# Kernel tuning notes

Hardware: AMD Instinct MI355X
Metric: run time of the kernel (lower is better)

## Reference

```python
import jax, jax.numpy as jnp
import numpy as np

B = 4096
IN_FEATS = 1024
OUT_FEATS = 1024
NUM_HEADS = 16
NUM_MEMS = 4096
HEAD_DIM = OUT_FEATS // NUM_HEADS
TEMPERATURE = 1.0
EPS = 0.0  # original code uses plain jnp.linalg.norm (no eps)


def setup_inputs() -> dict:
    key = jax.random.key(0)
    k1, k2, k3 = jax.random.split(key, 3)
    x = jax.random.normal(k1, (B, IN_FEATS), dtype=jnp.float32)
    # eqx.nn.Linear stores weight as [out, in]; uniform-like init replaced with normal scaled
    W_q = jax.random.normal(k2, (OUT_FEATS, IN_FEATS), dtype=jnp.float32) * (1.0 / np.sqrt(IN_FEATS))
    memories = jax.random.normal(k3, (NUM_HEADS, NUM_MEMS, HEAD_DIM), dtype=jnp.float32) * 0.02
    return {"x": x, "W_q": W_q, "memories": memories}


def reference(x, W_q, memories):
    # q = query_proj(x): [B, out_feats] -> [B, H, d]
    q = (x @ W_q.T).reshape(B, NUM_HEADS, HEAD_DIM)
    # L2-normalize queries and memories along feature dim
    q_norm = q / jnp.linalg.norm(q, axis=-1, keepdims=True)
    mem_norm = memories / jnp.linalg.norm(memories, axis=-1, keepdims=True)
    # cosine-similarity scores: [B, H, M]
    attn_scores = jnp.einsum('bhd,hmd->bhm', q_norm, mem_norm)
    # soft readout (hard=False branch)
    mem_probs = jax.nn.softmax(attn_scores / TEMPERATURE, axis=-1)
    # weighted combine of normalized memories, scaled by sqrt(head_dim)
    out = jnp.einsum('bhm,hmd->bhd', mem_probs, mem_norm) * jnp.sqrt(HEAD_DIM).astype(x.dtype)
    return out.reshape(B, OUT_FEATS)
```

## Files before the change

### kernel.cpp

```cpp
#include <hip/hip_runtime.h>
#include <stdint.h>

#define B_SZ  4096
#define HEADS 16
#define HD    64
#define M_SZ  4096
#define K_IN  1024
#define SW    72
#define LOG2E 1.44269504088896f

typedef _Float16 f16;
typedef f16  f16x2 __attribute__((ext_vector_type(2)));
typedef f16  f16x4 __attribute__((ext_vector_type(4)));
typedef f16  f16x8 __attribute__((ext_vector_type(8)));
typedef float f32x4 __attribute__((ext_vector_type(4)));

union U8 { uint4 u4; f16x8 h8; unsigned int ui[4]; unsigned short us[8]; };

__device__ __forceinline__ unsigned short f2h(float f) {
    _Float16 h = (_Float16)f;
    return __builtin_bit_cast(unsigned short, h);
}
__device__ __forceinline__ f16x8 ldsv8(const unsigned short* p) {
    U8 u; u.u4 = *reinterpret_cast<const uint4*>(p); return u.h8;
}

#if __has_builtin(__builtin_amdgcn_exp2f)
#define EXP2F(x) __builtin_amdgcn_exp2f(x)
#else
#define EXP2F(x) __expf((x) * 0.6931471805599453f)
#endif

__device__ __forceinline__ void gload_lds16(const void* g, void* l) {
    __builtin_amdgcn_global_load_lds(
        (const __attribute__((address_space(1))) void*)g,
        (__attribute__((address_space(3))) void*)l, 16, 0, 0);
}

__global__ __launch_bounds__(256) void k_conv(const float* __restrict__ x,
                                              const float* __restrict__ Wq,
                                              unsigned short* __restrict__ xh,
                                              unsigned short* __restrict__ Wh) {
    const int b = blockIdx.x;
    const float* src;
    unsigned short* dst;
    size_t base;
    if (b < 2048) { src = x;  dst = xh; base = (size_t)b * 2048; }
    else          { src = Wq; dst = Wh; base = (size_t)(b - 2048) * 2048; }
    const size_t i = base + (size_t)threadIdx.x * 8;
    float4 f0 = reinterpret_cast<const float4*>(src + i)[0];
    float4 f1 = reinterpret_cast<const float4*>(src + i)[1];
    U8 u;
    u.us[0] = f2h(f0.x); u.us[1] = f2h(f0.y); u.us[2] = f2h(f0.z); u.us[3] = f2h(f0.w);
    u.us[4] = f2h(f1.x); u.us[5] = f2h(f1.y); u.us[6] = f2h(f1.z); u.us[7] = f2h(f1.w);
    *reinterpret_cast<uint4*>(dst + i) = u.u4;
}

__global__ __launch_bounds__(256) void k_prep_mem(const float* __restrict__ mem,
                                                  unsigned short* __restrict__ F) {
    __shared__ float part[64][4];
    __shared__ float scale[64];
    __shared__ unsigned short Tn[64 * SW];

    const int h  = blockIdx.y;
    const int tl = blockIdx.x;
    const int m0 = tl * 64;
    const int tid = threadIdx.x;
    const int r = tid >> 2;
    const int c = tid & 3;

    const float* src = mem + ((size_t)(h * M_SZ + m0 + r)) * HD + c * 16;
    float v[16];
    float ss = 0.f;
#pragma unroll
    for (int i = 0; i < 4; i++) {
        float4 f = reinterpret_cast<const float4*>(src)[i];
        v[4*i+0] = f.x; v[4*i+1] = f.y; v[4*i+2] = f.z; v[4*i+3] = f.w;
        ss += f.x*f.x + f.y*f.y + f.z*f.z + f.w*f.w;
    }
    part[r][c] = ss;
    __syncthreads();
    if (tid < 64) {
        float s = part[tid][0] + part[tid][1] + part[tid][2] + part[tid][3];
        scale[tid] = rsqrtf(s);
    }
    __syncthreads();
    const float sc = scale[r];

    U8 a, b;
#pragma unroll
    for (int i = 0; i < 8; i++) { a.us[i] = f2h(v[i] * sc); b.us[i] = f2h(v[8 + i] * sc); }
    *reinterpret_cast<uint4*>(&Tn[r * SW + c * 16])     = a.u4;
    *reinterpret_cast<uint4*>(&Tn[r * SW + c * 16 + 8]) = b.u4;
    __syncthreads();

    const int w = tid >> 6, lane = tid & 63;
    const int l15 = lane & 15, quad = lane >> 4;
    unsigned short* Fd = F + ((size_t)(h * 64 + tl) * 16) * 512;

#pragma unroll
    for (int i = 0; i < 2; i++) {
        const int ch = w * 2 + i, g = ch >> 1, s = ch & 1;
        const int mp = 32 * (g >> 1) + ((l15 >> 2) * 8) + 4 * (g & 1) + (l15 & 3);
        uint4 vv = *reinterpret_cast<const uint4*>(&Tn[mp * SW + s * 32 + quad * 8]);
        *reinterpret_cast<uint4*>(Fd + ch * 512 + lane * 8) = vv;
    }
#pragma unroll
    for (int i = 0; i < 2; i++) {
        const int c2 = w * 2 + i, p = c2 >> 2, n = c2 & 3;
        U8 u;
#pragma unroll
        for (int j = 0; j < 8; j++)
            u.us[j] = Tn[(32 * p + quad * 8 + j) * SW + n * 16 + l15];
        *reinterpret_cast<uint4*>(Fd + (8 + c2) * 512 + lane * 8) = u.u4;
    }
}

__global__ __launch_bounds__(256, 2) void k_qproj(const unsigned short* __restrict__ xh,
                                                  const unsigned short* __restrict__ Wh,
                                                  unsigned short* __restrict__ qn) {
    __shared__ unsigned short As[128 * SW];
    __shared__ unsigned short Bs[64 * SW];

    const int b0 = blockIdx.x * 128;
    const int n0 = blockIdx.y * 64;
    const int t = threadIdx.x;
    const int w = t >> 6, lane = t & 63;
    const int l15 = lane & 15, quad = lane >> 4;

    f32x4 acc[2][4] = {};

    for (int kb = 0; kb < K_IN; kb += 64) {
        __syncthreads();
        {
            const unsigned short* px = xh + (size_t)(b0 + (t >> 1)) * K_IN + kb + (t & 1) * 32;
            const unsigned short* pw = Wh + (size_t)(n0 + (t >> 2)) * K_IN + kb + (t & 3) * 16;
            uint4 av[4];
#pragma unroll
            for (int i = 0; i < 4; i++) av[i] = reinterpret_cast<const uint4*>(px)[i];
            uint4 bv[2];
#pragma unroll
            for (int i = 0; i < 2; i++) bv[i] = reinterpret_cast<const uint4*>(pw)[i];
#pragma unroll
            for (int i = 0; i < 4; i++)
                *reinterpret_cast<uint4*>(&As[(t >> 1) * SW + (t & 1) * 32 + i * 8]) = av[i];
#pragma unroll
            for (int i = 0; i < 2; i++)
                *reinterpret_cast<uint4*>(&Bs[(t >> 2) * SW + (t & 3) * 16 + i * 8]) = bv[i];
        }
        __syncthreads();

#pragma unroll
        for (int s = 0; s < 2; s++) {
            f16x8 af[2];
#pragma unroll
            for (int qg = 0; qg < 2; qg++)
                af[qg] = ldsv8(&As[(w * 32 + qg * 16 + l15) * SW + s * 32 + quad * 8]);
#pragma unroll
            for (int g = 0; g < 4; g++) {
                f16x8 bf_ = ldsv8(&Bs[(g * 16 + l15) * SW + s * 32 + quad * 8]);
#pragma unroll
                for (int qg = 0; qg < 2; qg++)
                    acc[qg][g] = __builtin_amdgcn_mfma_f32_16x16x32_f16(af[qg], bf_, acc[qg][g], 0, 0, 0);
            }
        }
    }

    __syncthreads();
    unsigned short* Ct = As;
#pragma unroll
    for (int qg = 0; qg < 2; qg++) {
        float ssq[4];
#pragma unroll
        for (int r = 0; r < 4; r++) {
            float s = 0.f;
#pragma unroll
            for (int g = 0; g < 4; g++) s += acc[qg][g][r] * acc[qg][g][r];
            ssq[r] = s;
        }
#pragma unroll
        for (int mask = 1; mask <= 8; mask <<= 1)
#pragma unroll
            for (int r = 0; r < 4; r++) ssq[r] += __shfl_xor(ssq[r], mask, 64);
#pragma unroll
        for (int r = 0; r < 4; r++) {
            float inv = rsqrtf(ssq[r]) * LOG2E;
#pragma unroll
            for (int g = 0; g < 4; g++)
                Ct[(w * 32 + qg * 16 + quad * 4 + r) * SW + g * 16 + l15] = f2h(acc[qg][g][r] * inv);
        }
    }
    __syncthreads();

    const int row = t >> 1, half = (t & 1) * 32;
    unsigned short* dq = qn + (size_t)(b0 + row) * 1024 + n0 + half;
#pragma unroll
    for (int i = 0; i < 4; i++)
        reinterpret_cast<uint4*>(dq)[i] = *reinterpret_cast<const uint4*>(&Ct[row * SW + half + i * 8]);
}

__global__ __launch_bounds__(256, 2) void k_attn(const unsigned short* __restrict__ qn,
                                                 const unsigned short* __restrict__ F,
                                                 float* __restrict__ out) {
    __shared__ unsigned short buf[4][8192];

    const int b = blockIdx.x;
    const int h  = 2 * (b & 7) + (b >> 8);
    const int b0 = ((b >> 3) & 31) * 128;
    const int t = threadIdx.x;
    const int w = t >> 6, lane = t & 63;
    const int l15 = lane & 15, quad = lane >> 4;

    const f32x4 Z = {0.f, 0.f, 0.f, 0.f};

    f16x8 qf[2][2];
#pragma unroll
    for (int qg = 0; qg < 2; qg++)
#pragma unroll
        for (int s = 0; s < 2; s++) {
            U8 u;
            u.u4 = *reinterpret_cast<const uint4*>(
                qn + (size_t)(b0 + w * 32 + qg * 16 + l15) * 1024 + h * 64 + s * 32 + quad * 8);
            qf[qg][s] = u.h8;
        }

    const unsigned short* Fh = F + (size_t)h * 64 * 8192;

    f32x4 accO[2][4] = {};
    float lsum[2] = {0.f, 0.f};

    f16x8 puA[2][2], puB[2][2];
    f16x8 bwA[8],   bwB[8];

#if __has_builtin(__builtin_amdgcn_fdot2)
    const f16x2 one2 = {(_Float16)1.f, (_Float16)1.f};
#define LSUM4(qgi, puv)                                                          \
    {                                                                            \
        float s_ = lsum[qgi];                                                    \
        s_ = __builtin_amdgcn_fdot2(__builtin_bit_cast(f16x2, (puv).ui[0]), one2, s_, false); \
        s_ = __builtin_amdgcn_fdot2(__builtin_bit_cast(f16x2, (puv).ui[1]), one2, s_, false); \
        s_ = __builtin_amdgcn_fdot2(__builtin_bit_cast(f16x2, (puv).ui[2]), one2, s_, false); \
        s_ = __builtin_amdgcn_fdot2(__builtin_bit_cast(f16x2, (puv).ui[3]), one2, s_, false); \
        lsum[qgi] = s_;                                                          \
    }
#else
#define LSUM4(qgi, puv)                                                          \
    {                                                                            \
        float a0 = (float)(puv).h8[0] + (float)(puv).h8[1];                      \
        float a1 = (float)(puv).h8[2] + (float)(puv).h8[3];                      \
        float a2 = (float)(puv).h8[4] + (float)(puv).h8[5];                      \
        float a3 = (float)(puv).h8[6] + (float)(puv).h8[7];                      \
        lsum[qgi] += (a0 + a1) + (a2 + a3);                                      \
    }
#endif

#pragma unroll
    for (int tp = 0; tp < 3; tp++)
#pragma unroll
        for (int i = 0; i < 4; i++) {
            const int ch = w * 4 + i;
            gload_lds16(Fh + (size_t)tp * 8192 + ch * 512 + lane * 8, &buf[tp][ch * 512]);
        }
    __syncthreads();
    {
        f16x8 am[8];
#pragma unroll
        for (int ch = 0; ch < 8; ch++) am[ch] = ldsv8(&buf[0][ch * 512 + lane * 8]);
#pragma unroll
        for (int ch = 0; ch < 8; ch++) bwA[ch] = ldsv8(&buf[0][(8 + ch) * 512 + lane * 8]);
#pragma unroll
        for (int g = 0; g < 4; g++) {
            const int qg = g >> 1, p = g & 1;
            f32x4 t0 = __builtin_amdgcn_mfma_f32_16x16x32_f16(am[4*p+0], qf[qg][0], Z, 0, 0, 0);
            t0 = __builtin_amdgcn_mfma_f32_16x16x32_f16(am[4*p+1], qf[qg][1], t0, 0, 0, 0);
            f32x4 t1 = __builtin_amdgcn_mfma_f32_16x16x32_f16(am[4*p+2], qf[qg][0], Z, 0, 0, 0);
            t1 = __builtin_amdgcn_mfma_f32_16x16x32_f16(am[4*p+3], qf[qg][1], t1, 0, 0, 0);
            float p0 = EXP2F(t0[0]), p1 = EXP2F(t0[1]), p2 = EXP2F(t0[2]), p3 = EXP2F(t0[3]);
            float p4 = EXP2F(t1[0]), p5 = EXP2F(t1[1]), p6 = EXP2F(t1[2]), p7 = EXP2F(t1[3]);
            U8 pu;
#if __has_builtin(__builtin_amdgcn_cvt_pkrtz)
            pu.ui[0] = __builtin_bit_cast(unsigned int, __builtin_amdgcn_cvt_pkrtz(p0, p1));
            pu.ui[1] = __builtin_bit_cast(unsigned int, __builtin_amdgcn_cvt_pkrtz(p2, p3));
            pu.ui[2] = __builtin_bit_cast(unsigned int, __builtin_amdgcn_cvt_pkrtz(p4, p5));
            pu.ui[3] = __builtin_bit_cast(unsigned int, __builtin_amdgcn_cvt_pkrtz(p6, p7));
#else
            pu.us[0]=f2h(p0); pu.us[1]=f2h(p1); pu.us[2]=f2h(p2); pu.us[3]=f2h(p3);
            pu.us[4]=f2h(p4); pu.us[5]=f2h(p5); pu.us[6]=f2h(p6); pu.us[7]=f2h(p7);
#endif
            LSUM4(qg, pu);
            puA[qg][p] = pu.h8;
        }
    }

    auto body = [&](int tl, f16x8 (&puC)[2][2], f16x8 (&bwC)[8],
                            f16x8 (&puN)[2][2], f16x8 (&bwN)[8]) {
        const unsigned short* lb = buf[(tl + 1) & 3];
        f16x8 amn[8];
#pragma unroll
        for (int ch = 0; ch < 8; ch++) amn[ch] = ldsv8(&lb[ch * 512 + lane * 8]);
#pragma unroll
        for (int ch = 0; ch < 8; ch++) bwN[ch] = ldsv8(&lb[(8 + ch) * 512 + lane * 8]);
        if (tl + 3 < 64) {
            const unsigned short* gsrc = Fh + (size_t)(tl + 3) * 8192;
#pragma unroll
            for (int i = 0; i < 4; i++) {
                const int ch = w * 4 + i;
                gload_lds16(gsrc + ch * 512 + lane * 8, &buf[(tl + 3) & 3][ch * 512]);
            }
        }

        f32x4 sa[4], sb[4];
        auto expPack = [&](int g) {
            const int qg = g >> 1, p = g & 1;
            float p0 = EXP2F(sa[g][0]), p1 = EXP2F(sa[g][1]), p2 = EXP2F(sa[g][2]), p3 = EXP2F(sa[g][3]);
            float p4 = EXP2F(sb[g][0]), p5 = EXP2F(sb[g][1]), p6 = EXP2F(sb[g][2]), p7 = EXP2F(sb[g][3]);
            U8 pu;
#if __has_builtin(__builtin_amdgcn_cvt_pkrtz)
            pu.ui[0] = __builtin_bit_cast(unsigned int, __builtin_amdgcn_cvt_pkrtz(p0, p1));
            pu.ui[1] = __builtin_bit_cast(unsigned int, __builtin_amdgcn_cvt_pkrtz(p2, p3));
            pu.ui[2] = __builtin_bit_cast(unsigned int, __builtin_amdgcn_cvt_pkrtz(p4, p5));
            pu.ui[3] = __builtin_bit_cast(unsigned int, __builtin_amdgcn_cvt_pkrtz(p6, p7));
#else
            pu.us[0]=f2h(p0); pu.us[1]=f2h(p1); pu.us[2]=f2h(p2); pu.us[3]=f2h(p3);
            pu.us[4]=f2h(p4); pu.us[5]=f2h(p5); pu.us[6]=f2h(p6); pu.us[7]=f2h(p7);
#endif
            LSUM4(qg, pu);
            puN[qg][p] = pu.h8;
        };

#pragma unroll
        for (int g = 0; g < 4; g++) {
            const int qg = g >> 1, p = g & 1;
            __builtin_amdgcn_s_setprio(1);
            f32x4 t0 = __builtin_amdgcn_mfma_f32_16x16x32_f16(amn[4*p+0], qf[qg][0], Z, 0, 0, 0);
            t0 = __builtin_amdgcn_mfma_f32_16x16x32_f16(amn[4*p+1], qf[qg][1], t0, 0, 0, 0);
            f32x4 t1 = __builtin_amdgcn_mfma_f32_16x16x32_f16(amn[4*p+2], qf[qg][0], Z, 0, 0, 0);
            t1 = __builtin_amdgcn_mfma_f32_16x16x32_f16(amn[4*p+3], qf[qg][1], t1, 0, 0, 0);
            sa[g] = t0; sb[g] = t1;
#pragma unroll
            for (int n = 0; n < 4; n++)
                accO[qg][n] = __builtin_amdgcn_mfma_f32_16x16x32_f16(puC[qg][p], bwC[p * 4 + n], accO[qg][n], 0, 0, 0);
            __builtin_amdgcn_s_setprio(0);
            if (g >= 1) expPack(g - 1);
        }
        expPack(3);
    };

    for (int tt = 0; tt < 31; ++tt) {
        __syncthreads();
        body(2 * tt,     puA, bwA, puB, bwB);
        body(2 * tt + 1, puB, bwB, puA, bwA);
    }
    __syncthreads();
    body(62, puA, bwA, puB, bwB);

#pragma unroll
    for (int g = 0; g < 4; g++) {
        const int qg = g >> 1, p = g & 1;
#pragma unroll
        for (int n = 0; n < 4; n++)
            accO[qg][n] = __builtin_amdgcn_mfma_f32_16x16x32_f16(puB[qg][p], bwB[p * 4 + n], accO[qg][n], 0, 0, 0);
    }

#pragma unroll
    for (int qg = 0; qg < 2; qg++) {
        float s = lsum[qg];
        s += __shfl_xor(s, 16, 64);
        s += __shfl_xor(s, 32, 64);
        float inv = 8.0f / s;
#pragma unroll
        for (int r = 0; r < 4; r++) {
            float iv = __shfl(inv, quad * 4 + r, 64);
            float* po = out + (size_t)(b0 + w * 32 + qg * 16 + quad * 4 + r) * 1024 + h * 64;
#pragma unroll
            for (int n = 0; n < 4; n++)
                po[n * 16 + l15] = accO[qg][n][r] * iv;
        }
    }
}

extern "C" void kernel_launch(void* const* d_in, const int* in_sizes, int n_in,
                              void* d_out, int out_size, void* d_ws, size_t ws_size,
                              hipStream_t stream) {
    (void)in_sizes; (void)n_in; (void)out_size; (void)ws_size;
    const float* x   = (const float*)d_in[0];
    const float* Wq  = (const float*)d_in[1];
    const float* mem = (const float*)d_in[2];
    float* out = (float*)d_out;

    unsigned short* qn = (unsigned short*)d_ws;
    unsigned short* F  = qn + (size_t)B_SZ * 1024;
    unsigned short* xh = F  + (size_t)HEADS * 64 * 16 * 512;
    unsigned short* Wh = xh + (size_t)B_SZ * K_IN;

    k_conv    <<<2560, 256, 0, stream>>>(x, Wq, xh, Wh);
    k_prep_mem<<<dim3(64, 16), 256, 0, stream>>>(mem, F);
    k_qproj   <<<dim3(32, 16), 256, 0, stream>>>(xh, Wh, qn);
    k_attn    <<<512, 256, 0, stream>>>(qn, F, out);
}
```

Before: 175.3 us.

## Fuse fp16 conversion into qproj and merge memory prep into one launch

Removes the separate fp32-to-fp16 conversion kernel by having the query-projection GEMM load fp32 x and W_q directly and pack to fp16 while staging into LDS. Memory normalization blocks and qproj blocks are merged into a single launch using block-index ranges, cutting two launches and the intermediate xh/Wh round trip through global memory. The GEMM now reads twice the bytes per tile from global memory (fp32) and does conversion per tile, and W_q is re-converted by every row block.

```diff
diff --git a/kernel.cpp b/kernel.cpp
--- a/kernel.cpp
+++ b/kernel.cpp
@@ -31,100 +31,94 @@
 #define EXP2F(x) __expf((x) * 0.6931471805599453f)
 #endif
 
+#if __has_builtin(__builtin_amdgcn_cvt_pkrtz)
+#define PK2(a, b) __builtin_bit_cast(unsigned int, __builtin_amdgcn_cvt_pkrtz((a), (b)))
+#else
+__device__ __forceinline__ unsigned int PK2(float a, float b) {
+    return (unsigned int)f2h(a) | ((unsigned int)f2h(b) << 16);
+}
+#endif
+
 __device__ __forceinline__ void gload_lds16(const void* g, void* l) {
     __builtin_amdgcn_global_load_lds(
         (const __attribute__((address_space(1))) void*)g,
         (__attribute__((address_space(3))) void*)l, 16, 0, 0);
 }
 
-__global__ __launch_bounds__(256) void k_conv(const float* __restrict__ x,
-                                              const float* __restrict__ Wq,
-                                              unsigned short* __restrict__ xh,
-                                              unsigned short* __restrict__ Wh) {
+__global__ __launch_bounds__(256, 2) void k_fused(const float* __restrict__ x,
+                                                  const float* __restrict__ Wq,
+                                                  const float* __restrict__ mem,
+                                                  unsigned short* __restrict__ F,
+                                                  unsigned short* __restrict__ qn) {
+    __shared__ __align__(16) unsigned char smem[27648];
     const int b = blockIdx.x;
-    const float* src;
-    unsigned short* dst;
-    size_t base;
-    if (b < 2048) { src = x;  dst = xh; base = (size_t)b * 2048; }
-    else          { src = Wq; dst = Wh; base = (size_t)(b - 2048) * 2048; }
-    const size_t i = base + (size_t)threadIdx.x * 8;
-    float4 f0 = reinterpret_cast<const float4*>(src + i)[0];
-    float4 f1 = reinterpret_cast<const float4*>(src + i)[1];
-    U8 u;
-    u.us[0] = f2h(f0.x); u.us[1] = f2h(f0.y); u.us[2] = f2h(f0.z); u.us[3] = f2h(f0.w);
-    u.us[4] = f2h(f1.x); u.us[5] = f2h(f1.y); u.us[6] = f2h(f1.z); u.us[7] = f2h(f1.w);
-    *reinterpret_cast<uint4*>(dst + i) = u.u4;
-}
-
-__global__ __launch_bounds__(256) void k_prep_mem(const float* __restrict__ mem,
-                                                  unsigned short* __restrict__ F) {
-    __shared__ float part[64][4];
-    __shared__ float scale[64];
-    __shared__ unsigned short Tn[64 * SW];
-
-    const int h  = blockIdx.y;
-    const int tl = blockIdx.x;
-    const int m0 = tl * 64;
-    const int tid = threadIdx.x;
-    const int r = tid >> 2;
-    const int c = tid & 3;
-
-    const float* src = mem + ((size_t)(h * M_SZ + m0 + r)) * HD + c * 16;
-    float v[16];
-    float ss = 0.f;
-#pragma unroll
-    for (int i = 0; i < 4; i++) {
-        float4 f = reinterpret_cast<const float4*>(src)[i];
-        v[4*i+0] = f.x; v[4*i+1] = f.y; v[4*i+2] = f.z; v[4*i+3] = f.w;
-        ss += f.x*f.x + f.y*f.y + f.z*f.z + f.w*f.w;
-    }
-    part[r][c] = ss;
-    __syncthreads();
-    if (tid < 64) {
-        float s = part[tid][0] + part[tid][1] + part[tid][2] + part[tid][3];
-        scale[tid] = rsqrtf(s);
-    }
-    __syncthreads();
-    const float sc = scale[r];
-
-    U8 a, b;
-#pragma unroll
-    for (int i = 0; i < 8; i++) { a.us[i] = f2h(v[i] * sc); b.us[i] = f2h(v[8 + i] * sc); }
-    *reinterpret_cast<uint4*>(&Tn[r * SW + c * 16])     = a.u4;
-    *reinterpret_cast<uint4*>(&Tn[r * SW + c * 16 + 8]) = b.u4;
-    __syncthreads();
-
-    const int w = tid >> 6, lane = tid & 63;
-    const int l15 = lane & 15, quad = lane >> 4;
-    unsigned short* Fd = F + ((size_t)(h * 64 + tl) * 16) * 512;
-
-#pragma unroll
-    for (int i = 0; i < 2; i++) {
-        const int ch = w * 2 + i, g = ch >> 1, s = ch & 1;
-        const int mp = 32 * (g >> 1) + ((l15 >> 2) * 8) + 4 * (g & 1) + (l15 & 3);
-        uint4 vv = *reinterpret_cast<const uint4*>(&Tn[mp * SW + s * 32 + quad * 8]);
-        *reinterpret_cast<uint4*>(Fd + ch * 512 + lane * 8) = vv;
-    }
-#pragma unroll
-    for (int i = 0; i < 2; i++) {
-        const int c2 = w * 2 + i, p = c2 >> 2, n = c2 & 3;
-        U8 u;
-#pragma unroll
-        for (int j = 0; j < 8; j++)
-            u.us[j] = Tn[(32 * p + quad * 8 + j) * SW + n * 16 + l15];
-        *reinterpret_cast<uint4*>(Fd + (8 + c2) * 512 + lane * 8) = u.u4;
-    }
-}
-
-__global__ __launch_bounds__(256, 2) void k_qproj(const unsigned short* __restrict__ xh,
-                                                  const unsigned short* __restrict__ Wh,
-                                                  unsigned short* __restrict__ qn) {
-    __shared__ unsigned short As[128 * SW];
-    __shared__ unsigned short Bs[64 * SW];
-
-    const int b0 = blockIdx.x * 128;
-    const int n0 = blockIdx.y * 64;
     const int t = threadIdx.x;
+
+    if (b < 1024) {
+        float* part  = reinterpret_cast<float*>(smem);
+        float* scale = part + 256;
+        unsigned short* Tn = reinterpret_cast<unsigned short*>(scale + 64);
+
+        const int h  = b >> 6;
+        const int tl = b & 63;
+        const int m0 = tl * 64;
+        const int r = t >> 2;
+        const int c = t & 3;
+
+        const float* src = mem + ((size_t)(h * M_SZ + m0 + r)) * HD + c * 16;
+        float v[16];
+        float ss = 0.f;
+#pragma unroll
+        for (int i = 0; i < 4; i++) {
+            float4 f = reinterpret_cast<const float4*>(src)[i];
+            v[4*i+0] = f.x; v[4*i+1] = f.y; v[4*i+2] = f.z; v[4*i+3] = f.w;
+            ss += f.x*f.x + f.y*f.y + f.z*f.z + f.w*f.w;
+        }
+        part[r * 4 + c] = ss;
+        __syncthreads();
+        if (t < 64) {
+            float s = part[t*4+0] + part[t*4+1] + part[t*4+2] + part[t*4+3];
+            scale[t] = rsqrtf(s);
+        }
+        __syncthreads();
+        const float sc = scale[r];
+
+        U8 a2, b2;
+#pragma unroll
+        for (int i = 0; i < 8; i++) { a2.us[i] = f2h(v[i] * sc); b2.us[i] = f2h(v[8 + i] * sc); }
+        *reinterpret_cast<uint4*>(&Tn[r * SW + c * 16])     = a2.u4;
+        *reinterpret_cast<uint4*>(&Tn[r * SW + c * 16 + 8]) = b2.u4;
+        __syncthreads();
+
+        const int w = t >> 6, lane = t & 63;
+        const int l15 = lane & 15, quad = lane >> 4;
+        unsigned short* Fd = F + ((size_t)(h * 64 + tl) * 16) * 512;
+
+#pragma unroll
+        for (int i = 0; i < 2; i++) {
+            const int ch = w * 2 + i, g = ch >> 1, s = ch & 1;
+            const int mp = 32 * (g >> 1) + ((l15 >> 2) * 8) + 4 * (g & 1) + (l15 & 3);
+            uint4 vv = *reinterpret_cast<const uint4*>(&Tn[mp * SW + s * 32 + quad * 8]);
+            *reinterpret_cast<uint4*>(Fd + ch * 512 + lane * 8) = vv;
+        }
+#pragma unroll
+        for (int i = 0; i < 2; i++) {
+            const int c2 = w * 2 + i, p = c2 >> 2, n = c2 & 3;
+            U8 u;
+#pragma unroll
+            for (int j = 0; j < 8; j++)
+                u.us[j] = Tn[(32 * p + quad * 8 + j) * SW + n * 16 + l15];
+            *reinterpret_cast<uint4*>(Fd + (8 + c2) * 512 + lane * 8) = u.u4;
+        }
+        return;
+    }
+
+    unsigned short* As = reinterpret_cast<unsigned short*>(smem);
+    unsigned short* Bs = As + 128 * SW;
+
+    const int bq = b - 1024;
+    const int b0 = (bq & 31) * 128;
+    const int n0 = (bq >> 5) * 64;
     const int w = t >> 6, lane = t & 63;
     const int l15 = lane & 15, quad = lane >> 4;
 
@@ -133,20 +127,32 @@
     for (int kb = 0; kb < K_IN; kb += 64) {
         __syncthreads();
         {
-            const unsigned short* px = xh + (size_t)(b0 + (t >> 1)) * K_IN + kb + (t & 1) * 32;
-            const unsigned short* pw = Wh + (size_t)(n0 + (t >> 2)) * K_IN + kb + (t & 3) * 16;
-            uint4 av[4];
-#pragma unroll
-            for (int i = 0; i < 4; i++) av[i] = reinterpret_cast<const uint4*>(px)[i];
-            uint4 bv[2];
-#pragma unroll
-            for (int i = 0; i < 2; i++) bv[i] = reinterpret_cast<const uint4*>(pw)[i];
-#pragma unroll
-            for (int i = 0; i < 4; i++)
-                *reinterpret_cast<uint4*>(&As[(t >> 1) * SW + (t & 1) * 32 + i * 8]) = av[i];
-#pragma unroll
-            for (int i = 0; i < 2; i++)
-                *reinterpret_cast<uint4*>(&Bs[(t >> 2) * SW + (t & 3) * 16 + i * 8]) = bv[i];
+            const float* px = x  + (size_t)(b0 + (t >> 1)) * K_IN + kb + (t & 1) * 32;
+            const float* pw = Wq + (size_t)(n0 + (t >> 2)) * K_IN + kb + (t & 3) * 16;
+            float4 av[8];
+#pragma unroll
+            for (int i = 0; i < 8; i++) av[i] = reinterpret_cast<const float4*>(px)[i];
+            float4 bv[4];
+#pragma unroll
+            for (int i = 0; i < 4; i++) bv[i] = reinterpret_cast<const float4*>(pw)[i];
+#pragma unroll
+            for (int i = 0; i < 4; i++) {
+                U8 u;
+                u.ui[0] = PK2(av[2*i].x,   av[2*i].y);
+                u.ui[1] = PK2(av[2*i].z,   av[2*i].w);
+                u.ui[2] = PK2(av[2*i+1].x, av[2*i+1].y);
+                u.ui[3] = PK2(av[2*i+1].z, av[2*i+1].w);
+                *reinterpret_cast<uint4*>(&As[(t >> 1) * SW + (t & 1) * 32 + i * 8]) = u.u4;
+            }
+#pragma unroll
+            for (int i = 0; i < 2; i++) {
+                U8 u;
+                u.ui[0] = PK2(bv[2*i].x,   bv[2*i].y);
+                u.ui[1] = PK2(bv[2*i].z,   bv[2*i].w);
+                u.ui[2] = PK2(bv[2*i+1].x, bv[2*i+1].y);
+                u.ui[3] = PK2(bv[2*i+1].z, bv[2*i+1].w);
+                *reinterpret_cast<uint4*>(&Bs[(t >> 2) * SW + (t & 3) * 16 + i * 8]) = u.u4;
+            }
         }
         __syncthreads();
 
@@ -278,15 +284,10 @@
             float p0 = EXP2F(t0[0]), p1 = EXP2F(t0[1]), p2 = EXP2F(t0[2]), p3 = EXP2F(t0[3]);
             float p4 = EXP2F(t1[0]), p5 = EXP2F(t1[1]), p6 = EXP2F(t1[2]), p7 = EXP2F(t1[3]);
             U8 pu;
-#if __has_builtin(__builtin_amdgcn_cvt_pkrtz)
-            pu.ui[0] = __builtin_bit_cast(unsigned int, __builtin_amdgcn_cvt_pkrtz(p0, p1));
-            pu.ui[1] = __builtin_bit_cast(unsigned int, __builtin_amdgcn_cvt_pkrtz(p2, p3));
-            pu.ui[2] = __builtin_bit_cast(unsigned int, __builtin_amdgcn_cvt_pkrtz(p4, p5));
-            pu.ui[3] = __builtin_bit_cast(unsigned int, __builtin_amdgcn_cvt_pkrtz(p6, p7));
-#else
-            pu.us[0]=f2h(p0); pu.us[1]=f2h(p1); pu.us[2]=f2h(p2); pu.us[3]=f2h(p3);
-            pu.us[4]=f2h(p4); pu.us[5]=f2h(p5); pu.us[6]=f2h(p6); pu.us[7]=f2h(p7);
-#endif
+            pu.ui[0] = PK2(p0, p1);
+            pu.ui[1] = PK2(p2, p3);
+            pu.ui[2] = PK2(p4, p5);
+            pu.ui[3] = PK2(p6, p7);
             LSUM4(qg, pu);
             puA[qg][p] = pu.h8;
         }
@@ -315,15 +316,10 @@
             float p0 = EXP2F(sa[g][0]), p1 = EXP2F(sa[g][1]), p2 = EXP2F(sa[g][2]), p3 = EXP2F(sa[g][3]);
             float p4 = EXP2F(sb[g][0]), p5 = EXP2F(sb[g][1]), p6 = EXP2F(sb[g][2]), p7 = EXP2F(sb[g][3]);
             U8 pu;
-#if __has_builtin(__builtin_amdgcn_cvt_pkrtz)
-            pu.ui[0] = __builtin_bit_cast(unsigned int, __builtin_amdgcn_cvt_pkrtz(p0, p1));
-            pu.ui[1] = __builtin_bit_cast(unsigned int, __builtin_amdgcn_cvt_pkrtz(p2, p3));
-            pu.ui[2] = __builtin_bit_cast(unsigned int, __builtin_amdgcn_cvt_pkrtz(p4, p5));
-            pu.ui[3] = __builtin_bit_cast(unsigned int, __builtin_amdgcn_cvt_pkrtz(p6, p7));
-#else
-            pu.us[0]=f2h(p0); pu.us[1]=f2h(p1); pu.us[2]=f2h(p2); pu.us[3]=f2h(p3);
-            pu.us[4]=f2h(p4); pu.us[5]=f2h(p5); pu.us[6]=f2h(p6); pu.us[7]=f2h(p7);
-#endif
+            pu.ui[0] = PK2(p0, p1);
+            pu.ui[1] = PK2(p2, p3);
+            pu.ui[2] = PK2(p4, p5);
+            pu.ui[3] = PK2(p6, p7);
             LSUM4(qg, pu);
             puN[qg][p] = pu.h8;
         };
@@ -390,11 +386,7 @@
 
     unsigned short* qn = (unsigned short*)d_ws;
     unsigned short* F  = qn + (size_t)B_SZ * 1024;
-    unsigned short* xh = F  + (size_t)HEADS * 64 * 16 * 512;
-    unsigned short* Wh = xh + (size_t)B_SZ * K_IN;
-
-    k_conv    <<<2560, 256, 0, stream>>>(x, Wq, xh, Wh);
-    k_prep_mem<<<dim3(64, 16), 256, 0, stream>>>(mem, F);
-    k_qproj   <<<dim3(32, 16), 256, 0, stream>>>(xh, Wh, qn);
-    k_attn    <<<512, 256, 0, stream>>>(qn, F, out);
-}
+
+    k_fused<<<1536, 256, 0, stream>>>(x, Wq, mem, F, qn);
+    k_attn <<<512,  256, 0, stream>>>(qn, F, out);
+}
```

Result: slower. 207.9 us (+18.6%).
